# Performance work log

Hardware: AMD Instinct MI355X
Metric: run time of the kernel (lower is better)

Reference implementation:

```python
import jax, jax.numpy as jnp
import numpy as np

NEG_INF = -1e30  # masked_softmax fill (squad util convention)


def setup_inputs() -> dict:
    key = jax.random.key(0)
    ks = jax.random.split(key, 5)
    B, S, H = 4, 2048, 512
    x = jax.random.normal(ks[0], (B, S, H), dtype=jnp.float32)
    mask = jax.random.randint(ks[1], (B, S), 0, 2, dtype=jnp.int32)
    mask = mask.at[:, 0].set(1)  # ensure at least one valid key per row
    W_comb = jax.random.normal(ks[2], (H, 3 * H), dtype=jnp.float32) * (1.0 / np.sqrt(H))
    b_comb = jnp.zeros((3 * H,), dtype=jnp.float32)
    W_out = jax.random.normal(ks[3], (H, H), dtype=jnp.float32) * (1.0 / np.sqrt(H))
    b_out = jnp.zeros((H,), dtype=jnp.float32)
    return {"x": x, "mask": mask, "W_comb": W_comb, "b_comb": b_comb,
            "W_out": W_out, "b_out": b_out}


def reference(x, mask, W_comb, b_comb, W_out, b_out):
    B, S, H = x.shape
    n_head = 8
    d = H // n_head
    scale = d ** 0.5
    qkv = x @ W_comb + b_comb                      # [B,S,3H]
    q, k, v = jnp.split(qkv, 3, axis=-1)
    q = q.reshape(B, S, n_head, d)
    k = k.reshape(B, S, n_head, d)
    v = v.reshape(B, S, n_head, d)
    # [B,h,Sq,Sk] scores; mask applies along the key axis
    scores = jnp.einsum('bqhd,bkhd->bhqk', q / scale, k)
    key_mask = (mask > 0)[:, None, None, :]        # [B,1,1,Sk]
    logits = jnp.where(key_mask, scores, NEG_INF)
    attn = jax.nn.softmax(logits, axis=-1)         # dropout = identity (eval)
    out = jnp.einsum('bhqk,bkhd->bqhd', attn, v).reshape(B, S, H)
    return out @ W_out + b_out
```

## Files before the change

### kernel.cpp

```cpp
#include <hip/hip_runtime.h>
#include <hip/hip_bf16.h>
#include <stdint.h>

typedef unsigned short u16;
typedef unsigned int u32;
typedef __attribute__((ext_vector_type(8))) __bf16 bf16x8;
typedef __attribute__((ext_vector_type(8))) unsigned short us8;
typedef __attribute__((ext_vector_type(4))) unsigned short us4;
typedef __attribute__((ext_vector_type(4))) float f32x4;
typedef __attribute__((ext_vector_type(16))) float f32x16;
typedef __attribute__((ext_vector_type(4))) unsigned int u32x4;
typedef __attribute__((ext_vector_type(2))) unsigned int u32x2;

#define KSCALE_Q 0.18033688011112042f

#define VMCNT(n) asm volatile("s_waitcnt vmcnt(" #n ")" ::: "memory")
#define BARRIER() __builtin_amdgcn_s_barrier()

__device__ inline u16 f2bf(float f) {
  union { __bf16 b; u16 s; } x; x.b = (__bf16)f; return x.s;
}
__device__ inline u32 packbf(float a, float b) {
  return (u32)f2bf(a) | ((u32)f2bf(b) << 16);
}
__device__ inline f32x16 zero16() {
  f32x16 z; for (int i = 0; i < 16; ++i) z[i] = 0.f; return z;
}
__device__ __forceinline__ void gl_lds16(const u16* g, u16* l) {
  __builtin_amdgcn_global_load_lds(
      (const __attribute__((address_space(1))) void*)g,
      (__attribute__((address_space(3))) void*)l, 16, 0, 0);
}
__device__ __forceinline__ void pl32swap(u32& a, u32& b) {
#if __has_builtin(__builtin_amdgcn_permlane32_swap)
  u32x2 r = __builtin_amdgcn_permlane32_swap(a, b, false, false);
  a = r[0]; b = r[1];
#else
  u32 ta = (u32)__shfl_xor((int)a, 32);
  u32 tb = (u32)__shfl_xor((int)b, 32);
  int hi = (threadIdx.x & 63) >> 5;
  u32 na = hi ? tb : a;
  u32 nb = hi ? b : ta;
  a = na; b = nb;
#endif
}

__global__ __launch_bounds__(256) void prep(
    const float* __restrict__ x, const float* __restrict__ Wc,
    const float* __restrict__ Wo, const int* __restrict__ mask,
    u16* __restrict__ xbf, u16* __restrict__ wct, u16* __restrict__ wot,
    int* __restrict__ idx, int* __restrict__ nbv) {
  int r = blockIdx.x, tid = threadIdx.x;
  if (r < 4096) {
    int i = r * 256 + tid;
    float4 v = ((const float4*)x)[i];
    us4 o;
    o[0] = f2bf(v.x); o[1] = f2bf(v.y); o[2] = f2bf(v.z); o[3] = f2bf(v.w);
    ((us4*)xbf)[i] = o;
    return;
  }
  __shared__ float tile[32][33];
  __shared__ int ps[256];
  if (r < 5120) {
    const float* in; u16* outT; int R, C, bi;
    if (r < 4864) { in = Wc; outT = wct; R = 512; C = 1536; bi = r - 4096; }
    else          { in = Wo; outT = wot; R = 512; C = 512;  bi = r - 4864; }
    int nbx = C >> 5;
    int bx = bi % nbx, by = bi / nbx;
    int xq = tid & 31, yq = tid >> 5;
    int c0 = bx * 32, r0 = by * 32;
    for (int j = 0; j < 32; j += 8)
      tile[yq + j][xq] = in[(size_t)(r0 + yq + j) * C + c0 + xq];
    __syncthreads();
    for (int j = 0; j < 32; j += 8)
      outT[(size_t)(c0 + yq + j) * R + r0 + xq] = f2bf(tile[xq][yq + j]);
    return;
  }
  int b = r - 5120;
  const int* mrow = mask + b * 2048;
  int4 a = ((const int4*)mrow)[tid * 2];
  int4 c = ((const int4*)mrow)[tid * 2 + 1];
  int v[8] = {a.x, a.y, a.z, a.w, c.x, c.y, c.z, c.w};
  int cnt = 0;
  for (int i = 0; i < 8; ++i) cnt += (v[i] > 0);
  ps[tid] = cnt;
  __syncthreads();
  for (int off = 1; off < 256; off <<= 1) {
    int xv = ps[tid];
    int yv = (tid >= off) ? ps[tid - off] : 0;
    __syncthreads();
    ps[tid] = xv + yv;
    __syncthreads();
  }
  int total = ps[255];
  int pos = ps[tid] - cnt;
  int* ip = idx + b * 2048;
  for (int i = 0; i < 8; ++i)
    if (v[i] > 0) ip[pos++] = tid * 8 + i;
  for (int i = 0; i < 8; ++i) {
    int j = tid * 8 + i;
    if (j >= total) ip[j] = 0;
  }
  if (tid == 0) nbv[b] = total;
}

__global__ __launch_bounds__(256) void gemm_qkv(
    const u16* __restrict__ A, const u16* __restrict__ Bt,
    const float* __restrict__ bias, u16* __restrict__ Qc,
    u16* __restrict__ Kc, u16* __restrict__ VTc,
    const int* __restrict__ idx, const int* __restrict__ nbv) {
  const int K = 512;
  int bid = blockIdx.x;
  bool isQ = bid < 256;
  int b = 0, m0, n0;
  if (isQ) {
    m0 = (bid >> 2) * 128;
    n0 = (bid & 3) * 128;
  } else {
    int t = bid - 256;
    b = t >> 7;
    int rr_ = t & 127;
    m0 = (rr_ & 15) * 128;
    n0 = (rr_ >> 4) * 128 + 512;
    int npad = (nbv[b] + 127) & ~127;
    if (m0 >= npad) return;
  }
  __shared__ __align__(16) u16 As[2][128 * 64];
  __shared__ __align__(16) u16 Bs[2][128 * 64];
  int tid = threadIdx.x, wave = tid >> 6, lane = tid & 63;
  int quad = lane >> 4, l16 = lane & 15;
  int wm = (wave >> 1) * 64, wn = (wave & 1) * 64;

  int r8 = lane >> 3;
  int cb = (lane & 7) ^ r8;
  const u16* agp[4];
  for (int i = 0; i < 4; ++i) {
    int row = m0 + wave * 32 + i * 8 + r8;
    int grow = isQ ? row : (b * 2048 + idx[b * 2048 + row]);
    agp[i] = A + (size_t)grow * K + cb * 8;
  }
  const u16* bg = Bt + (size_t)(n0 + wave * 32 + r8) * K + cb * 8;
  int lofs = (wave * 32) * 64 + lane * 8;

  f32x4 acc[4][4];
  for (int i = 0; i < 4; ++i)
    for (int j = 0; j < 4; ++j) acc[i][j] = (f32x4){0.f, 0.f, 0.f, 0.f};

  int rx = l16 & 7;

  auto stage = [&](int buf, int kk) {
    u16* al = As[buf] + lofs;
    u16* bl = Bs[buf] + lofs;
#pragma unroll
    for (int i = 0; i < 4; ++i)
      gl_lds16(agp[i] + kk, al + i * 8 * 64);
#pragma unroll
    for (int i = 0; i < 4; ++i)
      gl_lds16(bg + kk + (size_t)(i * 8) * K, bl + i * 8 * 64);
  };

  stage(0, 0);
  for (int t = 0; t < 8; ++t) {
    if (t < 7) { stage((t + 1) & 1, (t + 1) * 64); VMCNT(8); }
    else       { VMCNT(0); }
    BARRIER();
    const u16* Asb = As[t & 1];
    const u16* Bsb = Bs[t & 1];
#pragma unroll
    for (int ks = 0; ks < 2; ++ks) {
      int pos = ((ks * 4 + quad) ^ rx) * 8;
      bf16x8 af[4], bfr[4];
#pragma unroll
      for (int i = 0; i < 4; ++i)
        af[i] = *(const bf16x8*)(Asb + (wm + i * 16 + l16) * 64 + pos);
#pragma unroll
      for (int j = 0; j < 4; ++j)
        bfr[j] = *(const bf16x8*)(Bsb + (wn + j * 16 + l16) * 64 + pos);
#pragma unroll
      for (int i = 0; i < 4; ++i)
#pragma unroll
        for (int j = 0; j < 4; ++j)
          acc[i][j] = __builtin_amdgcn_mfma_f32_16x16x32_bf16(
              af[i], bfr[j], acc[i][j], 0, 0, 0);
    }
    BARRIER();
  }
  for (int j = 0; j < 4; ++j) {
    int col = n0 + wn + j * 16 + l16;
    float bv = bias[col];
    if (isQ) {
      for (int i = 0; i < 4; ++i) {
        int rowb = m0 + wm + i * 16 + quad * 4;
        for (int rr = 0; rr < 4; ++rr)
          Qc[(size_t)(rowb + rr) * 512 + col] =
              f2bf((acc[i][j][rr] + bv) * KSCALE_Q);
      }
    } else if (col < 1024) {
      int ck = col - 512;
      for (int i = 0; i < 4; ++i) {
        int key0 = m0 + wm + i * 16 + quad * 4;
        for (int rr = 0; rr < 4; ++rr)
          Kc[((size_t)b * 2048 + key0 + rr) * 512 + ck] =
              f2bf(acc[i][j][rr] + bv);
      }
    } else {
      int hd = col - 1024;
      int h = hd >> 6, d = hd & 63;
      u16* vrow = VTc + ((size_t)(b * 8 + h) * 64 + d) * 2048;
      for (int i = 0; i < 4; ++i) {
        int key0 = m0 + wm + i * 16 + quad * 4;
        us4 pk;
        for (int rr = 0; rr < 4; ++rr) pk[rr] = f2bf(acc[i][j][rr] + bv);
        *(us4*)(vrow + key0) = pk;
      }
    }
  }
}

__global__ __launch_bounds__(256) void gemm_out(
    const u16* __restrict__ A, const u16* __restrict__ Bt,
    const float* __restrict__ bias, float* __restrict__ Cout) {
  const int K = 512, N = 512;
  int m0 = blockIdx.y * 128, n0 = blockIdx.x * 128;
  __shared__ __align__(16) u16 As[2][128 * 64];
  __shared__ __align__(16) u16 Bs[2][128 * 64];
  int tid = threadIdx.x, wave = tid >> 6, lane = tid & 63;
  int quad = lane >> 4, l16 = lane & 15;
  int wm = (wave >> 1) * 64, wn = (wave & 1) * 64;

  int r8 = lane >> 3;
  int cb = (lane & 7) ^ r8;
  const u16* ag = A + (size_t)(m0 + wave * 32 + r8) * K + cb * 8;
  const u16* bg = Bt + (size_t)(n0 + wave * 32 + r8) * K + cb * 8;
  int lofs = (wave * 32) * 64 + lane * 8;

  f32x4 acc[4][4];
  for (int i = 0; i < 4; ++i)
    for (int j = 0; j < 4; ++j) acc[i][j] = (f32x4){0.f, 0.f, 0.f, 0.f};

  int rx = l16 & 7;

  auto stage = [&](int buf, int kk) {
    u16* al = As[buf] + lofs;
    u16* bl = Bs[buf] + lofs;
#pragma unroll
    for (int i = 0; i < 4; ++i)
      gl_lds16(ag + kk + (size_t)(i * 8) * K, al + i * 8 * 64);
#pragma unroll
    for (int i = 0; i < 4; ++i)
      gl_lds16(bg + kk + (size_t)(i * 8) * K, bl + i * 8 * 64);
  };

  stage(0, 0);
  for (int t = 0; t < 8; ++t) {
    if (t < 7) { stage((t + 1) & 1, (t + 1) * 64); VMCNT(8); }
    else       { VMCNT(0); }
    BARRIER();
    const u16* Asb = As[t & 1];
    const u16* Bsb = Bs[t & 1];
#pragma unroll
    for (int ks = 0; ks < 2; ++ks) {
      int pos = ((ks * 4 + quad) ^ rx) * 8;
      bf16x8 af[4], bfr[4];
#pragma unroll
      for (int i = 0; i < 4; ++i)
        af[i] = *(const bf16x8*)(Asb + (wm + i * 16 + l16) * 64 + pos);
#pragma unroll
      for (int j = 0; j < 4; ++j)
        bfr[j] = *(const bf16x8*)(Bsb + (wn + j * 16 + l16) * 64 + pos);
#pragma unroll
      for (int i = 0; i < 4; ++i)
#pragma unroll
        for (int j = 0; j < 4; ++j)
          acc[i][j] = __builtin_amdgcn_mfma_f32_16x16x32_bf16(
              af[i], bfr[j], acc[i][j], 0, 0, 0);
    }
    BARRIER();
  }
  for (int j = 0; j < 4; ++j) {
    int col = n0 + wn + j * 16 + l16;
    float bv = bias[col];
    for (int i = 0; i < 4; ++i) {
      int rowb = m0 + wm + i * 16 + quad * 4;
      for (int rr = 0; rr < 4; ++rr)
        Cout[(size_t)(rowb + rr) * N + col] = acc[i][j][rr] + bv;
    }
  }
}

__global__ __launch_bounds__(256, 2) void attn_kernel(
    const u16* __restrict__ Qc, const u16* __restrict__ Kc,
    const u16* __restrict__ VTc, const int* __restrict__ nbv,
    u16* __restrict__ aout) {
  int flat = blockIdx.x;
  int xcd = flat & 7, ii = flat >> 3;
  int p = ((ii >> 4) << 3) | xcd;
  int c = ii & 15;
  int b = p >> 3, h = p & 7, q0 = c * 128;
  int bh = b * 8 + h;
  int tid = threadIdx.x, wave = tid >> 6, lane = tid & 63;
  int l5 = lane & 31, hi = lane >> 5;
  int nb = nbv[b];
  int npad = (nb + 127) & ~127;
  int NT = npad >> 7;

  __shared__ __align__(16) u16 Kt[2][128 * 64];
  __shared__ __align__(16) u16 Vt[2][64 * 128];

  bf16x8 qf[4];
  int qrow = b * 2048 + q0 + wave * 32 + l5;
#pragma unroll
  for (int s = 0; s < 4; ++s)
    qf[s] = *(const bf16x8*)(Qc + (size_t)qrow * 512 + h * 64 + s * 16 +
                             hi * 8);
  VMCNT(0);

  f32x16 o[2];
  o[0] = zero16(); o[1] = zero16();
  float lsum = 0.f;

  int krr = lane >> 3;
  int kcb = (lane & 7) ^ krr;
  const u16* kg = Kc + ((size_t)(b * 2048) + wave * 32 + krr) * 512 + h * 64 +
                  kcb * 8;
  int vrr = lane >> 4;

  auto stageKV = [&](int buf, int kt0) {
    u16* kl = Kt[buf] + (wave * 32) * 64 + lane * 8;
#pragma unroll
    for (int i = 0; i < 4; ++i)
      gl_lds16(kg + (size_t)(kt0 + i * 8) * 512, kl + i * 8 * 64);
    u16* vl = Vt[buf] + (wave * 16) * 128 + lane * 8;
#pragma unroll
    for (int i = 0; i < 4; ++i) {
      int vr = wave * 16 + i * 4 + vrr;
      int vcb = (lane & 15) ^ (vr & 15);
      gl_lds16(VTc + ((size_t)(bh * 64) + vr) * 2048 + kt0 + vcb * 8,
               vl + i * 4 * 128);
    }
  };

  int rx = l5 & 7;
  stageKV(0, 0);
  for (int t = 0; t < NT; ++t) {
    if (t + 1 < NT) { stageKV((t + 1) & 1, (t + 1) * 128); VMCNT(8); }
    else            { VMCNT(0); }
    BARRIER();
    const u16* Ktc = Kt[t & 1];
    const u16* Vtc = Vt[t & 1];
    int kt0 = t * 128;
    bool maskT = (kt0 + 128 > nb);

#pragma unroll
    for (int kp = 0; kp < 2; ++kp) {
      bf16x8 ka[2][4];
#pragma unroll
      for (int cc = 0; cc < 2; ++cc) {
        const u16* kro = Ktc + ((kp * 2 + cc) * 32 + l5) * 64;
#pragma unroll
        for (int s = 0; s < 4; ++s)
          ka[cc][s] = *(const bf16x8*)(kro + ((s * 2 + hi) ^ rx) * 8);
      }
      f32x16 sa[2];
      sa[0] = zero16(); sa[1] = zero16();
#pragma unroll
      for (int s = 0; s < 4; ++s) {
        sa[0] = __builtin_amdgcn_mfma_f32_32x32x16_bf16(ka[0][s], qf[s],
                                                        sa[0], 0, 0, 0);
        sa[1] = __builtin_amdgcn_mfma_f32_32x32x16_bf16(ka[1][s], qf[s],
                                                        sa[1], 0, 0, 0);
      }
      bf16x8 pb[2][2];
#pragma unroll
      for (int cc = 0; cc < 2; ++cc) {
        int kg4 = kp * 2 + cc;
        if (maskT) {
#pragma unroll
          for (int r = 0; r < 16; ++r) {
            int jg = kt0 + kg4 * 32 + (r & 3) + 8 * (r >> 2) + 4 * hi;
            if (jg >= nb) sa[cc][r] = -1e30f;
          }
        }
        u32 pk[8];
        float ls = 0.f;
#pragma unroll
        for (int j = 0; j < 8; ++j) {
          float e0 = __builtin_amdgcn_exp2f(sa[cc][2 * j]);
          float e1 = __builtin_amdgcn_exp2f(sa[cc][2 * j + 1]);
          ls += e0 + e1;
          pk[j] = packbf(e0, e1);
        }
        lsum += ls;
#pragma unroll
        for (int t2 = 0; t2 < 2; ++t2) {
          u32 a0 = pk[t2 * 4 + 0], a2 = pk[t2 * 4 + 2];
          u32 a1 = pk[t2 * 4 + 1], a3 = pk[t2 * 4 + 3];
          pl32swap(a0, a2);
          pl32swap(a1, a3);
          u32x4 qv; qv[0] = a0; qv[1] = a1; qv[2] = a2; qv[3] = a3;
          pb[cc][t2] = __builtin_bit_cast(bf16x8, qv);
        }
      }
#pragma unroll
      for (int cc = 0; cc < 2; ++cc) {
        int kg4 = kp * 2 + cc;
#pragma unroll
        for (int t2 = 0; t2 < 2; ++t2) {
          int cblk = kg4 * 4 + t2 * 2 + hi;
#pragma unroll
          for (int dc = 0; dc < 2; ++dc) {
            int vrow = dc * 32 + l5;
            bf16x8 va = *(const bf16x8*)(Vtc + vrow * 128 +
                                         ((cblk ^ (vrow & 15)) * 8));
            o[dc] = __builtin_amdgcn_mfma_f32_32x32x16_bf16(
                va, pb[cc][t2], o[dc], 0, 0, 0);
          }
        }
      }
    }
    BARRIER();
  }

  float lt = lsum;
  lt += __shfl_xor(lt, 32);
  float inv = 1.f / lt;
#pragma unroll
  for (int dc = 0; dc < 2; ++dc)
#pragma unroll
    for (int mI = 0; mI < 4; ++mI) {
      us4 pk;
      for (int r = 0; r < 4; ++r) pk[r] = f2bf(o[dc][mI * 4 + r] * inv);
      *(us4*)(aout + (size_t)qrow * 512 + h * 64 + dc * 32 + mI * 8 +
              hi * 4) = pk;
    }
}

extern "C" void kernel_launch(void* const* d_in, const int* in_sizes, int n_in,
                              void* d_out, int out_size, void* d_ws,
                              size_t ws_size, hipStream_t stream) {
  const float* x = (const float*)d_in[0];
  const int* mask = (const int*)d_in[1];
  const float* Wc = (const float*)d_in[2];
  const float* bc = (const float*)d_in[3];
  const float* Wo = (const float*)d_in[4];
  const float* bo = (const float*)d_in[5];
  float* out = (float*)d_out;

  char* ws = (char*)d_ws;
  u16* xbf = (u16*)(ws);
  u16* wct = (u16*)(ws + 8388608);
  u16* wot = (u16*)(ws + 9961472);
  u16* Qc  = (u16*)(ws + 10485760);
  u16* Kc  = (u16*)(ws + 18874368);
  u16* vtc = (u16*)(ws + 27262976);
  int* idx = (int*)(ws + 35651584);
  int* nbv = (int*)(ws + 35684352);
  u16* aout = xbf;

  prep<<<5124, 256, 0, stream>>>(x, Wc, Wo, mask, xbf, wct, wot, idx, nbv);
  gemm_qkv<<<768, 256, 0, stream>>>(xbf, wct, bc, Qc, Kc, vtc, idx, nbv);
  attn_kernel<<<512, 256, 0, stream>>>(Qc, Kc, vtc, nbv, aout);
  gemm_out<<<dim3(4, 64), 256, 0, stream>>>(aout, wot, bo, out);
}
```

Before: 144.2 us.

## Fuse prep, QKV GEMM, attention and output GEMM into one persistent kernel

Replaces the four separate launches with a single 512-block persistent kernel. The stages are separated by atomic-counter grid barriers. The QKV and output GEMM tiles are handed out through an atomic work queue, and shared memory is one buffer reused by every stage. The aim is to remove the launch gaps and tail drain between kernels, at the cost of spin-wait barriers, a memset of the counters, and a kernel that relies on all 512 blocks being co-resident under a two-blocks-per-CU register bound.

Result: slower. 462.5 us (+220.7%).

```diff
diff --git a/kernel.cpp b/kernel.cpp
--- a/kernel.cpp
+++ b/kernel.cpp
@@ -5,7 +5,6 @@
 typedef unsigned short u16;
 typedef unsigned int u32;
 typedef __attribute__((ext_vector_type(8))) __bf16 bf16x8;
-typedef __attribute__((ext_vector_type(8))) unsigned short us8;
 typedef __attribute__((ext_vector_type(4))) unsigned short us4;
 typedef __attribute__((ext_vector_type(4))) float f32x4;
 typedef __attribute__((ext_vector_type(16))) float f32x16;
@@ -13,6 +12,7 @@
 typedef __attribute__((ext_vector_type(2))) unsigned int u32x2;
 
 #define KSCALE_Q 0.18033688011112042f
+#define NBLK 512
 
 #define VMCNT(n) asm volatile("s_waitcnt vmcnt(" #n ")" ::: "memory")
 #define BARRIER() __builtin_amdgcn_s_barrier()
@@ -45,72 +45,28 @@
 #endif
 }
 
-__global__ __launch_bounds__(256) void prep(
-    const float* __restrict__ x, const float* __restrict__ Wc,
-    const float* __restrict__ Wo, const int* __restrict__ mask,
-    u16* __restrict__ xbf, u16* __restrict__ wct, u16* __restrict__ wot,
-    int* __restrict__ idx, int* __restrict__ nbv) {
-  int r = blockIdx.x, tid = threadIdx.x;
-  if (r < 4096) {
-    int i = r * 256 + tid;
-    float4 v = ((const float4*)x)[i];
-    us4 o;
-    o[0] = f2bf(v.x); o[1] = f2bf(v.y); o[2] = f2bf(v.z); o[3] = f2bf(v.w);
-    ((us4*)xbf)[i] = o;
-    return;
-  }
-  __shared__ float tile[32][33];
-  __shared__ int ps[256];
-  if (r < 5120) {
-    const float* in; u16* outT; int R, C, bi;
-    if (r < 4864) { in = Wc; outT = wct; R = 512; C = 1536; bi = r - 4096; }
-    else          { in = Wo; outT = wot; R = 512; C = 512;  bi = r - 4864; }
-    int nbx = C >> 5;
-    int bx = bi % nbx, by = bi / nbx;
-    int xq = tid & 31, yq = tid >> 5;
-    int c0 = bx * 32, r0 = by * 32;
-    for (int j = 0; j < 32; j += 8)
-      tile[yq + j][xq] = in[(size_t)(r0 + yq + j) * C + c0 + xq];
-    __syncthreads();
-    for (int j = 0; j < 32; j += 8)
-      outT[(size_t)(c0 + yq + j) * R + r0 + xq] = f2bf(tile[xq][yq + j]);
-    return;
-  }
-  int b = r - 5120;
-  const int* mrow = mask + b * 2048;
-  int4 a = ((const int4*)mrow)[tid * 2];
-  int4 c = ((const int4*)mrow)[tid * 2 + 1];
-  int v[8] = {a.x, a.y, a.z, a.w, c.x, c.y, c.z, c.w};
-  int cnt = 0;
-  for (int i = 0; i < 8; ++i) cnt += (v[i] > 0);
-  ps[tid] = cnt;
+__device__ __forceinline__ void grid_barrier(int* ctr) {
   __syncthreads();
-  for (int off = 1; off < 256; off <<= 1) {
-    int xv = ps[tid];
-    int yv = (tid >= off) ? ps[tid - off] : 0;
-    __syncthreads();
-    ps[tid] = xv + yv;
-    __syncthreads();
-  }
-  int total = ps[255];
-  int pos = ps[tid] - cnt;
-  int* ip = idx + b * 2048;
-  for (int i = 0; i < 8; ++i)
-    if (v[i] > 0) ip[pos++] = tid * 8 + i;
-  for (int i = 0; i < 8; ++i) {
-    int j = tid * 8 + i;
-    if (j >= total) ip[j] = 0;
-  }
-  if (tid == 0) nbv[b] = total;
-}
-
-__global__ __launch_bounds__(256) void gemm_qkv(
-    const u16* __restrict__ A, const u16* __restrict__ Bt,
+  if (threadIdx.x == 0) {
+    __hip_atomic_fetch_add(ctr, 1, __ATOMIC_RELEASE,
+                           __HIP_MEMORY_SCOPE_AGENT);
+    for (long sp = 0; sp < (1L << 26); ++sp) {
+      int v = __hip_atomic_load(ctr, __ATOMIC_ACQUIRE,
+                                __HIP_MEMORY_SCOPE_AGENT);
+      if (v >= NBLK) break;
+      __builtin_amdgcn_s_sleep(2);
+    }
+  }
+  __syncthreads();
+  __threadfence();
+}
+
+__device__ __forceinline__ void do_qkv(
+    int bid, const u16* __restrict__ A, const u16* __restrict__ Bt,
     const float* __restrict__ bias, u16* __restrict__ Qc,
     u16* __restrict__ Kc, u16* __restrict__ VTc,
-    const int* __restrict__ idx, const int* __restrict__ nbv) {
+    const int* __restrict__ idx, const int* __restrict__ nbv, u16* smem) {
   const int K = 512;
-  int bid = blockIdx.x;
   bool isQ = bid < 256;
   int b = 0, m0, n0;
   if (isQ) {
@@ -125,8 +81,8 @@
     int npad = (nbv[b] + 127) & ~127;
     if (m0 >= npad) return;
   }
-  __shared__ __align__(16) u16 As[2][128 * 64];
-  __shared__ __align__(16) u16 Bs[2][128 * 64];
+  u16* As = smem;
+  u16* Bs = smem + 16384;
   int tid = threadIdx.x, wave = tid >> 6, lane = tid & 63;
   int quad = lane >> 4, l16 = lane & 15;
   int wm = (wave >> 1) * 64, wn = (wave & 1) * 64;
@@ -149,8 +105,8 @@
   int rx = l16 & 7;
 
   auto stage = [&](int buf, int kk) {
-    u16* al = As[buf] + lofs;
-    u16* bl = Bs[buf] + lofs;
+    u16* al = As + buf * 8192 + lofs;
+    u16* bl = Bs + buf * 8192 + lofs;
 #pragma unroll
     for (int i = 0; i < 4; ++i)
       gl_lds16(agp[i] + kk, al + i * 8 * 64);
@@ -164,8 +120,8 @@
     if (t < 7) { stage((t + 1) & 1, (t + 1) * 64); VMCNT(8); }
     else       { VMCNT(0); }
     BARRIER();
-    const u16* Asb = As[t & 1];
-    const u16* Bsb = Bs[t & 1];
+    const u16* Asb = As + (t & 1) * 8192;
+    const u16* Bsb = Bs + (t & 1) * 8192;
 #pragma unroll
     for (int ks = 0; ks < 2; ++ks) {
       int pos = ((ks * 4 + quad) ^ rx) * 8;
@@ -217,82 +173,10 @@
   }
 }
 
-__global__ __launch_bounds__(256) void gemm_out(
-    const u16* __restrict__ A, const u16* __restrict__ Bt,
-    const float* __restrict__ bias, float* __restrict__ Cout) {
-  const int K = 512, N = 512;
-  int m0 = blockIdx.y * 128, n0 = blockIdx.x * 128;
-  __shared__ __align__(16) u16 As[2][128 * 64];
-  __shared__ __align__(16) u16 Bs[2][128 * 64];
-  int tid = threadIdx.x, wave = tid >> 6, lane = tid & 63;
-  int quad = lane >> 4, l16 = lane & 15;
-  int wm = (wave >> 1) * 64, wn = (wave & 1) * 64;
-
-  int r8 = lane >> 3;
-  int cb = (lane & 7) ^ r8;
-  const u16* ag = A + (size_t)(m0 + wave * 32 + r8) * K + cb * 8;
-  const u16* bg = Bt + (size_t)(n0 + wave * 32 + r8) * K + cb * 8;
-  int lofs = (wave * 32) * 64 + lane * 8;
-
-  f32x4 acc[4][4];
-  for (int i = 0; i < 4; ++i)
-    for (int j = 0; j < 4; ++j) acc[i][j] = (f32x4){0.f, 0.f, 0.f, 0.f};
-
-  int rx = l16 & 7;
-
-  auto stage = [&](int buf, int kk) {
-    u16* al = As[buf] + lofs;
-    u16* bl = Bs[buf] + lofs;
-#pragma unroll
-    for (int i = 0; i < 4; ++i)
-      gl_lds16(ag + kk + (size_t)(i * 8) * K, al + i * 8 * 64);
-#pragma unroll
-    for (int i = 0; i < 4; ++i)
-      gl_lds16(bg + kk + (size_t)(i * 8) * K, bl + i * 8 * 64);
-  };
-
-  stage(0, 0);
-  for (int t = 0; t < 8; ++t) {
-    if (t < 7) { stage((t + 1) & 1, (t + 1) * 64); VMCNT(8); }
-    else       { VMCNT(0); }
-    BARRIER();
-    const u16* Asb = As[t & 1];
-    const u16* Bsb = Bs[t & 1];
-#pragma unroll
-    for (int ks = 0; ks < 2; ++ks) {
-      int pos = ((ks * 4 + quad) ^ rx) * 8;
-      bf16x8 af[4], bfr[4];
-#pragma unroll
-      for (int i = 0; i < 4; ++i)
-        af[i] = *(const bf16x8*)(Asb + (wm + i * 16 + l16) * 64 + pos);
-#pragma unroll
-      for (int j = 0; j < 4; ++j)
-        bfr[j] = *(const bf16x8*)(Bsb + (wn + j * 16 + l16) * 64 + pos);
-#pragma unroll
-      for (int i = 0; i < 4; ++i)
-#pragma unroll
-        for (int j = 0; j < 4; ++j)
-          acc[i][j] = __builtin_amdgcn_mfma_f32_16x16x32_bf16(
-              af[i], bfr[j], acc[i][j], 0, 0, 0);
-    }
-    BARRIER();
-  }
-  for (int j = 0; j < 4; ++j) {
-    int col = n0 + wn + j * 16 + l16;
-    float bv = bias[col];
-    for (int i = 0; i < 4; ++i) {
-      int rowb = m0 + wm + i * 16 + quad * 4;
-      for (int rr = 0; rr < 4; ++rr)
-        Cout[(size_t)(rowb + rr) * N + col] = acc[i][j][rr] + bv;
-    }
-  }
-}
-
-__global__ __launch_bounds__(256, 2) void attn_kernel(
-    const u16* __restrict__ Qc, const u16* __restrict__ Kc,
+__device__ __forceinline__ void do_attn(
+    int flat, const u16* __restrict__ Qc, const u16* __restrict__ Kc,
     const u16* __restrict__ VTc, const int* __restrict__ nbv,
-    u16* __restrict__ aout) {
-  int flat = blockIdx.x;
+    u16* __restrict__ aout, u16* smem) {
   int xcd = flat & 7, ii = flat >> 3;
   int p = ((ii >> 4) << 3) | xcd;
   int c = ii & 15;
@@ -304,8 +188,8 @@
   int npad = (nb + 127) & ~127;
   int NT = npad >> 7;
 
-  __shared__ __align__(16) u16 Kt[2][128 * 64];
-  __shared__ __align__(16) u16 Vt[2][64 * 128];
+  u16* Kt = smem;
+  u16* Vt = smem + 16384;
 
   bf16x8 qf[4];
   int qrow = b * 2048 + q0 + wave * 32 + l5;
@@ -326,11 +210,11 @@
   int vrr = lane >> 4;
 
   auto stageKV = [&](int buf, int kt0) {
-    u16* kl = Kt[buf] + (wave * 32) * 64 + lane * 8;
+    u16* kl = Kt + buf * 8192 + (wave * 32) * 64 + lane * 8;
 #pragma unroll
     for (int i = 0; i < 4; ++i)
       gl_lds16(kg + (size_t)(kt0 + i * 8) * 512, kl + i * 8 * 64);
-    u16* vl = Vt[buf] + (wave * 16) * 128 + lane * 8;
+    u16* vl = Vt + buf * 8192 + (wave * 16) * 128 + lane * 8;
 #pragma unroll
     for (int i = 0; i < 4; ++i) {
       int vr = wave * 16 + i * 4 + vrr;
@@ -346,8 +230,8 @@
     if (t + 1 < NT) { stageKV((t + 1) & 1, (t + 1) * 128); VMCNT(8); }
     else            { VMCNT(0); }
     BARRIER();
-    const u16* Ktc = Kt[t & 1];
-    const u16* Vtc = Vt[t & 1];
+    const u16* Ktc = Kt + (t & 1) * 8192;
+    const u16* Vtc = Vt + (t & 1) * 8192;
     int kt0 = t * 128;
     bool maskT = (kt0 + 128 > nb);
 
@@ -433,6 +317,172 @@
       *(us4*)(aout + (size_t)qrow * 512 + h * 64 + dc * 32 + mI * 8 +
               hi * 4) = pk;
     }
+}
+
+__device__ __forceinline__ void do_out(
+    int job, const u16* __restrict__ A, const u16* __restrict__ Bt,
+    const float* __restrict__ bias, float* __restrict__ Cout, u16* smem) {
+  const int K = 512, N = 512;
+  int m0 = (job >> 2) * 128, n0 = (job & 3) * 128;
+  u16* As = smem;
+  u16* Bs = smem + 16384;
+  int tid = threadIdx.x, wave = tid >> 6, lane = tid & 63;
+  int quad = lane >> 4, l16 = lane & 15;
+  int wm = (wave >> 1) * 64, wn = (wave & 1) * 64;
+
+  int r8 = lane >> 3;
+  int cb = (lane & 7) ^ r8;
+  const u16* ag = A + (size_t)(m0 + wave * 32 + r8) * K + cb * 8;
+  const u16* bg = Bt + (size_t)(n0 + wave * 32 + r8) * K + cb * 8;
+  int lofs = (wave * 32) * 64 + lane * 8;
+
+  f32x4 acc[4][4];
+  for (int i = 0; i < 4; ++i)
+    for (int j = 0; j < 4; ++j) acc[i][j] = (f32x4){0.f, 0.f, 0.f, 0.f};
+
+  int rx = l16 & 7;
+
+  auto stage = [&](int buf, int kk) {
+    u16* al = As + buf * 8192 + lofs;
+    u16* bl = Bs + buf * 8192 + lofs;
+#pragma unroll
+    for (int i = 0; i < 4; ++i)
+      gl_lds16(ag + kk + (size_t)(i * 8) * K, al + i * 8 * 64);
+#pragma unroll
+    for (int i = 0; i < 4; ++i)
+      gl_lds16(bg + kk + (size_t)(i * 8) * K, bl + i * 8 * 64);
+  };
+
+  stage(0, 0);
+  for (int t = 0; t < 8; ++t) {
+    if (t < 7) { stage((t + 1) & 1, (t + 1) * 64); VMCNT(8); }
+    else       { VMCNT(0); }
+    BARRIER();
+    const u16* Asb = As + (t & 1) * 8192;
+    const u16* Bsb = Bs + (t & 1) * 8192;
+#pragma unroll
+    for (int ks = 0; ks < 2; ++ks) {
+      int pos = ((ks * 4 + quad) ^ rx) * 8;
+      bf16x8 af[4], bfr[4];
+#pragma unroll
+      for (int i = 0; i < 4; ++i)
+        af[i] = *(const bf16x8*)(Asb + (wm + i * 16 + l16) * 64 + pos);
+#pragma unroll
+      for (int j = 0; j < 4; ++j)
+        bfr[j] = *(const bf16x8*)(Bsb + (wn + j * 16 + l16) * 64 + pos);
+#pragma unroll
+      for (int i = 0; i < 4; ++i)
+#pragma unroll
+        for (int j = 0; j < 4; ++j)
+          acc[i][j] = __builtin_amdgcn_mfma_f32_16x16x32_bf16(
+              af[i], bfr[j], acc[i][j], 0, 0, 0);
+    }
+    BARRIER();
+  }
+  for (int j = 0; j < 4; ++j) {
+    int col = n0 + wn + j * 16 + l16;
+    float bv = bias[col];
+    for (int i = 0; i < 4; ++i) {
+      int rowb = m0 + wm + i * 16 + quad * 4;
+      for (int rr = 0; rr < 4; ++rr)
+        Cout[(size_t)(rowb + rr) * N + col] = acc[i][j][rr] + bv;
+    }
+  }
+}
+
+__global__ __launch_bounds__(256, 2) void fused(
+    const float* __restrict__ x, const float* __restrict__ Wc,
+    const float* __restrict__ Wo, const int* __restrict__ mask,
+    const float* __restrict__ bc, const float* __restrict__ bo,
+    u16* __restrict__ xbf, u16* __restrict__ wct, u16* __restrict__ wot,
+    u16* __restrict__ Qc, u16* __restrict__ Kc, u16* __restrict__ VTc,
+    int* __restrict__ idx, int* __restrict__ nbv, float* __restrict__ out,
+    int* __restrict__ ctrs) {
+  __shared__ __align__(16) u16 smem[32768];
+  __shared__ int jobS;
+  int tid = threadIdx.x, blk = blockIdx.x;
+
+  {
+#pragma unroll
+    for (int t = 0; t < 8; ++t) {
+      int i = blk * 2048 + t * 256 + tid;
+      float4 v = ((const float4*)x)[i];
+      us4 o;
+      o[0] = f2bf(v.x); o[1] = f2bf(v.y); o[2] = f2bf(v.z); o[3] = f2bf(v.w);
+      ((us4*)xbf)[i] = o;
+    }
+  }
+  {
+    float* tile = (float*)smem;
+    for (int tj = blk; tj < 1024; tj += NBLK) {
+      const float* in; u16* outT; int R, C, bi;
+      if (tj < 768) { in = Wc; outT = wct; R = 512; C = 1536; bi = tj; }
+      else          { in = Wo; outT = wot; R = 512; C = 512;  bi = tj - 768; }
+      int nbx = C >> 5;
+      int bx = bi % nbx, by = bi / nbx;
+      int xq = tid & 31, yq = tid >> 5;
+      int c0 = bx * 32, r0 = by * 32;
+      for (int j = 0; j < 32; j += 8)
+        tile[(yq + j) * 33 + xq] = in[(size_t)(r0 + yq + j) * C + c0 + xq];
+      __syncthreads();
+      for (int j = 0; j < 32; j += 8)
+        outT[(size_t)(c0 + yq + j) * R + r0 + xq] =
+            f2bf(tile[xq * 33 + yq + j]);
+      __syncthreads();
+    }
+  }
+  if (blk < 4) {
+    int* ps = (int*)(smem + 4096);
+    int b = blk;
+    const int* mrow = mask + b * 2048;
+    int4 a = ((const int4*)mrow)[tid * 2];
+    int4 c = ((const int4*)mrow)[tid * 2 + 1];
+    int v[8] = {a.x, a.y, a.z, a.w, c.x, c.y, c.z, c.w};
+    int cnt = 0;
+    for (int i = 0; i < 8; ++i) cnt += (v[i] > 0);
+    ps[tid] = cnt;
+    __syncthreads();
+    for (int off = 1; off < 256; off <<= 1) {
+      int xv = ps[tid];
+      int yv = (tid >= off) ? ps[tid - off] : 0;
+      __syncthreads();
+      ps[tid] = xv + yv;
+      __syncthreads();
+    }
+    int total = ps[255];
+    int pos = ps[tid] - cnt;
+    int* ip = idx + b * 2048;
+    for (int i = 0; i < 8; ++i)
+      if (v[i] > 0) ip[pos++] = tid * 8 + i;
+    for (int i = 0; i < 8; ++i) {
+      int j = tid * 8 + i;
+      if (j >= total) ip[j] = 0;
+    }
+    if (tid == 0) nbv[b] = total;
+  }
+  grid_barrier(ctrs + 0);
+
+  for (;;) {
+    __syncthreads();
+    if (tid == 0) jobS = atomicAdd(ctrs + 4, 1);
+    __syncthreads();
+    int job = jobS;
+    if (job >= 768) break;
+    do_qkv(job, xbf, wct, bc, Qc, Kc, VTc, idx, nbv, smem);
+  }
+  grid_barrier(ctrs + 1);
+
+  do_attn(blk, Qc, Kc, VTc, nbv, xbf , smem);
+  grid_barrier(ctrs + 2);
+
+  for (;;) {
+    __syncthreads();
+    if (tid == 0) jobS = atomicAdd(ctrs + 5, 1);
+    __syncthreads();
+    int job = jobS;
+    if (job >= 256) break;
+    do_out(job, xbf, wot, bo, out, smem);
+  }
 }
 
 extern "C" void kernel_launch(void* const* d_in, const int* in_sizes, int n_in,
@@ -455,10 +505,9 @@
   u16* vtc = (u16*)(ws + 27262976);
   int* idx = (int*)(ws + 35651584);
   int* nbv = (int*)(ws + 35684352);
-  u16* aout = xbf;
-
-  prep<<<5124, 256, 0, stream>>>(x, Wc, Wo, mask, xbf, wct, wot, idx, nbv);
-  gemm_qkv<<<768, 256, 0, stream>>>(xbf, wct, bc, Qc, Kc, vtc, idx, nbv);
-  attn_kernel<<<512, 256, 0, stream>>>(Qc, Kc, vtc, nbv, aout);
-  gemm_out<<<dim3(4, 64), 256, 0, stream>>>(aout, wot, bo, out);
-}
+  int* ctrs = (int*)(ws + 35684416);
+
+  hipMemsetAsync(ctrs, 0, 32, stream);
+  fused<<<NBLK, 256, 0, stream>>>(x, Wc, Wo, mask, bc, bo, xbf, wct, wot,
+                                  Qc, Kc, vtc, idx, nbv, out, ctrs);
+}
```

## Halve attention KV tile to 64 keys, raise occupancy, split output GEMM tiles

Applied to the files above, without the earlier changes.

The attention kernel now stages 64-key K/V tiles instead of 128, which halves LDS per block, and raises launch bounds to allow 4 blocks per CU. It also wraps the MFMA sections in s_setprio so waves doing matrix work get priority. The output GEMM switches to 128x64 tiles on a 512-block 1D grid so more CUs are busy. The costs are more loop iterations and barriers per key and more A-tile reloads in the GEMM.

Result: slower. 148.9 us (+3.3%).

```diff
diff --git a/kernel.cpp b/kernel.cpp
--- a/kernel.cpp
+++ b/kernel.cpp
@@ -5,7 +5,6 @@
 typedef unsigned short u16;
 typedef unsigned int u32;
 typedef __attribute__((ext_vector_type(8))) __bf16 bf16x8;
-typedef __attribute__((ext_vector_type(8))) unsigned short us8;
 typedef __attribute__((ext_vector_type(4))) unsigned short us4;
 typedef __attribute__((ext_vector_type(4))) float f32x4;
 typedef __attribute__((ext_vector_type(16))) float f32x16;
@@ -217,43 +216,45 @@
   }
 }
 
-__global__ __launch_bounds__(256) void gemm_out(
+__global__ __launch_bounds__(256, 3) void gemm_out(
     const u16* __restrict__ A, const u16* __restrict__ Bt,
     const float* __restrict__ bias, float* __restrict__ Cout) {
   const int K = 512, N = 512;
-  int m0 = blockIdx.y * 128, n0 = blockIdx.x * 128;
+  int bid = blockIdx.x;
+  int m0 = (bid >> 3) * 128, n0 = (bid & 7) * 64;
   __shared__ __align__(16) u16 As[2][128 * 64];
-  __shared__ __align__(16) u16 Bs[2][128 * 64];
+  __shared__ __align__(16) u16 Bs[2][64 * 64];
   int tid = threadIdx.x, wave = tid >> 6, lane = tid & 63;
   int quad = lane >> 4, l16 = lane & 15;
-  int wm = (wave >> 1) * 64, wn = (wave & 1) * 64;
+  int wm = (wave >> 1) * 64, wn = (wave & 1) * 32;
 
   int r8 = lane >> 3;
   int cb = (lane & 7) ^ r8;
   const u16* ag = A + (size_t)(m0 + wave * 32 + r8) * K + cb * 8;
-  const u16* bg = Bt + (size_t)(n0 + wave * 32 + r8) * K + cb * 8;
-  int lofs = (wave * 32) * 64 + lane * 8;
-
-  f32x4 acc[4][4];
+  const u16* bg = Bt + (size_t)(n0 + wave * 16 + r8) * K + cb * 8;
+  int lofsA = (wave * 32) * 64 + lane * 8;
+  int lofsB = (wave * 16) * 64 + lane * 8;
+
+  f32x4 acc[4][2];
   for (int i = 0; i < 4; ++i)
-    for (int j = 0; j < 4; ++j) acc[i][j] = (f32x4){0.f, 0.f, 0.f, 0.f};
+    for (int j = 0; j < 2; ++j) acc[i][j] = (f32x4){0.f, 0.f, 0.f, 0.f};
 
   int rx = l16 & 7;
 
   auto stage = [&](int buf, int kk) {
-    u16* al = As[buf] + lofs;
-    u16* bl = Bs[buf] + lofs;
+    u16* al = As[buf] + lofsA;
+    u16* bl = Bs[buf] + lofsB;
 #pragma unroll
     for (int i = 0; i < 4; ++i)
       gl_lds16(ag + kk + (size_t)(i * 8) * K, al + i * 8 * 64);
 #pragma unroll
-    for (int i = 0; i < 4; ++i)
+    for (int i = 0; i < 2; ++i)
       gl_lds16(bg + kk + (size_t)(i * 8) * K, bl + i * 8 * 64);
   };
 
   stage(0, 0);
   for (int t = 0; t < 8; ++t) {
-    if (t < 7) { stage((t + 1) & 1, (t + 1) * 64); VMCNT(8); }
+    if (t < 7) { stage((t + 1) & 1, (t + 1) * 64); VMCNT(6); }
     else       { VMCNT(0); }
     BARRIER();
     const u16* Asb = As[t & 1];
@@ -261,23 +262,23 @@
 #pragma unroll
     for (int ks = 0; ks < 2; ++ks) {
       int pos = ((ks * 4 + quad) ^ rx) * 8;
-      bf16x8 af[4], bfr[4];
+      bf16x8 af[4], bfr[2];
 #pragma unroll
       for (int i = 0; i < 4; ++i)
         af[i] = *(const bf16x8*)(Asb + (wm + i * 16 + l16) * 64 + pos);
 #pragma unroll
-      for (int j = 0; j < 4; ++j)
+      for (int j = 0; j < 2; ++j)
         bfr[j] = *(const bf16x8*)(Bsb + (wn + j * 16 + l16) * 64 + pos);
 #pragma unroll
       for (int i = 0; i < 4; ++i)
 #pragma unroll
-        for (int j = 0; j < 4; ++j)
+        for (int j = 0; j < 2; ++j)
           acc[i][j] = __builtin_amdgcn_mfma_f32_16x16x32_bf16(
               af[i], bfr[j], acc[i][j], 0, 0, 0);
     }
     BARRIER();
   }
-  for (int j = 0; j < 4; ++j) {
+  for (int j = 0; j < 2; ++j) {
     int col = n0 + wn + j * 16 + l16;
     float bv = bias[col];
     for (int i = 0; i < 4; ++i) {
@@ -288,7 +289,7 @@
   }
 }
 
-__global__ __launch_bounds__(256, 2) void attn_kernel(
+__global__ __launch_bounds__(256, 4) void attn_kernel(
     const u16* __restrict__ Qc, const u16* __restrict__ Kc,
     const u16* __restrict__ VTc, const int* __restrict__ nbv,
     u16* __restrict__ aout) {
@@ -301,11 +302,10 @@
   int tid = threadIdx.x, wave = tid >> 6, lane = tid & 63;
   int l5 = lane & 31, hi = lane >> 5;
   int nb = nbv[b];
-  int npad = (nb + 127) & ~127;
-  int NT = npad >> 7;
-
-  __shared__ __align__(16) u16 Kt[2][128 * 64];
-  __shared__ __align__(16) u16 Vt[2][64 * 128];
+  int NT = ((nb + 63) & ~63) >> 6;
+
+  __shared__ __align__(16) u16 Kt[2][64 * 64];
+  __shared__ __align__(16) u16 Vt[2][64 * 64];
 
   bf16x8 qf[4];
   int qrow = b * 2048 + q0 + wave * 32 + l5;
@@ -319,105 +319,98 @@
   o[0] = zero16(); o[1] = zero16();
   float lsum = 0.f;
 
-  int krr = lane >> 3;
-  int kcb = (lane & 7) ^ krr;
-  const u16* kg = Kc + ((size_t)(b * 2048) + wave * 32 + krr) * 512 + h * 64 +
-                  kcb * 8;
-  int vrr = lane >> 4;
+  int rr8 = lane >> 3;
+  int cb8 = (lane & 7) ^ rr8;
+  const u16* kg = Kc + ((size_t)(b * 2048) + wave * 16 + rr8) * 512 + h * 64 +
+                  cb8 * 8;
+  const u16* vg = VTc + ((size_t)(bh * 64) + wave * 16 + rr8) * 2048 + cb8 * 8;
 
   auto stageKV = [&](int buf, int kt0) {
-    u16* kl = Kt[buf] + (wave * 32) * 64 + lane * 8;
-#pragma unroll
-    for (int i = 0; i < 4; ++i)
-      gl_lds16(kg + (size_t)(kt0 + i * 8) * 512, kl + i * 8 * 64);
-    u16* vl = Vt[buf] + (wave * 16) * 128 + lane * 8;
-#pragma unroll
-    for (int i = 0; i < 4; ++i) {
-      int vr = wave * 16 + i * 4 + vrr;
-      int vcb = (lane & 15) ^ (vr & 15);
-      gl_lds16(VTc + ((size_t)(bh * 64) + vr) * 2048 + kt0 + vcb * 8,
-               vl + i * 4 * 128);
-    }
+    u16* kl = Kt[buf] + (wave * 16) * 64 + lane * 8;
+    gl_lds16(kg + (size_t)kt0 * 512, kl);
+    gl_lds16(kg + (size_t)(kt0 + 8) * 512, kl + 8 * 64);
+    u16* vl = Vt[buf] + (wave * 16) * 64 + lane * 8;
+    gl_lds16(vg + kt0, vl);
+    gl_lds16(vg + kt0 + (size_t)8 * 2048, vl + 8 * 64);
   };
 
   int rx = l5 & 7;
   stageKV(0, 0);
   for (int t = 0; t < NT; ++t) {
-    if (t + 1 < NT) { stageKV((t + 1) & 1, (t + 1) * 128); VMCNT(8); }
+    if (t + 1 < NT) { stageKV((t + 1) & 1, (t + 1) * 64); VMCNT(4); }
     else            { VMCNT(0); }
     BARRIER();
     const u16* Ktc = Kt[t & 1];
     const u16* Vtc = Vt[t & 1];
-    int kt0 = t * 128;
-    bool maskT = (kt0 + 128 > nb);
-
-#pragma unroll
-    for (int kp = 0; kp < 2; ++kp) {
-      bf16x8 ka[2][4];
-#pragma unroll
-      for (int cc = 0; cc < 2; ++cc) {
-        const u16* kro = Ktc + ((kp * 2 + cc) * 32 + l5) * 64;
-#pragma unroll
-        for (int s = 0; s < 4; ++s)
-          ka[cc][s] = *(const bf16x8*)(kro + ((s * 2 + hi) ^ rx) * 8);
-      }
-      f32x16 sa[2];
-      sa[0] = zero16(); sa[1] = zero16();
-#pragma unroll
-      for (int s = 0; s < 4; ++s) {
-        sa[0] = __builtin_amdgcn_mfma_f32_32x32x16_bf16(ka[0][s], qf[s],
-                                                        sa[0], 0, 0, 0);
-        sa[1] = __builtin_amdgcn_mfma_f32_32x32x16_bf16(ka[1][s], qf[s],
-                                                        sa[1], 0, 0, 0);
-      }
-      bf16x8 pb[2][2];
-#pragma unroll
-      for (int cc = 0; cc < 2; ++cc) {
-        int kg4 = kp * 2 + cc;
-        if (maskT) {
-#pragma unroll
-          for (int r = 0; r < 16; ++r) {
-            int jg = kt0 + kg4 * 32 + (r & 3) + 8 * (r >> 2) + 4 * hi;
-            if (jg >= nb) sa[cc][r] = -1e30f;
-          }
+    int kt0 = t * 64;
+    bool maskT = (kt0 + 64 > nb);
+
+    bf16x8 ka[2][4];
+#pragma unroll
+    for (int cc = 0; cc < 2; ++cc) {
+      const u16* kro = Ktc + (cc * 32 + l5) * 64;
+#pragma unroll
+      for (int s = 0; s < 4; ++s)
+        ka[cc][s] = *(const bf16x8*)(kro + (((s * 2 + hi) ^ rx) * 8));
+    }
+    f32x16 sa[2];
+    sa[0] = zero16(); sa[1] = zero16();
+    __builtin_amdgcn_s_setprio(1);
+#pragma unroll
+    for (int s = 0; s < 4; ++s) {
+      sa[0] = __builtin_amdgcn_mfma_f32_32x32x16_bf16(ka[0][s], qf[s],
+                                                      sa[0], 0, 0, 0);
+      sa[1] = __builtin_amdgcn_mfma_f32_32x32x16_bf16(ka[1][s], qf[s],
+                                                      sa[1], 0, 0, 0);
+    }
+    __builtin_amdgcn_s_setprio(0);
+    bf16x8 pb[2][2];
+#pragma unroll
+    for (int cc = 0; cc < 2; ++cc) {
+      if (maskT) {
+#pragma unroll
+        for (int r = 0; r < 16; ++r) {
+          int jg = kt0 + cc * 32 + (r & 3) + 8 * (r >> 2) + 4 * hi;
+          if (jg >= nb) sa[cc][r] = -1e30f;
         }
-        u32 pk[8];
-        float ls = 0.f;
-#pragma unroll
-        for (int j = 0; j < 8; ++j) {
-          float e0 = __builtin_amdgcn_exp2f(sa[cc][2 * j]);
-          float e1 = __builtin_amdgcn_exp2f(sa[cc][2 * j + 1]);
-          ls += e0 + e1;
-          pk[j] = packbf(e0, e1);
+      }
+      u32 pk[8];
+      float ls = 0.f;
+#pragma unroll
+      for (int j = 0; j < 8; ++j) {
+        float e0 = __builtin_amdgcn_exp2f(sa[cc][2 * j]);
+        float e1 = __builtin_amdgcn_exp2f(sa[cc][2 * j + 1]);
+        ls += e0 + e1;
+        pk[j] = packbf(e0, e1);
+      }
+      lsum += ls;
+#pragma unroll
+      for (int t2 = 0; t2 < 2; ++t2) {
+        u32 a0 = pk[t2 * 4 + 0], a2 = pk[t2 * 4 + 2];
+        u32 a1 = pk[t2 * 4 + 1], a3 = pk[t2 * 4 + 3];
+        pl32swap(a0, a2);
+        pl32swap(a1, a3);
+        u32x4 qv; qv[0] = a0; qv[1] = a1; qv[2] = a2; qv[3] = a3;
+        pb[cc][t2] = __builtin_bit_cast(bf16x8, qv);
+      }
+    }
+    __builtin_amdgcn_s_setprio(1);
+#pragma unroll
+    for (int cc = 0; cc < 2; ++cc) {
+#pragma unroll
+      for (int t2 = 0; t2 < 2; ++t2) {
+        int cblk = cc * 4 + t2 * 2 + hi;
+#pragma unroll
+        for (int dc = 0; dc < 2; ++dc) {
+          int vrow = dc * 32 + l5;
+          bf16x8 va = *(const bf16x8*)(Vtc + vrow * 64 +
+                                       ((cblk ^ (vrow & 7)) * 8));
+          o[dc] = __builtin_amdgcn_mfma_f32_32x32x16_bf16(
+              va, pb[cc][t2], o[dc], 0, 0, 0);
         }
-        lsum += ls;
-#pragma unroll
-        for (int t2 = 0; t2 < 2; ++t2) {
-          u32 a0 = pk[t2 * 4 + 0], a2 = pk[t2 * 4 + 2];
-          u32 a1 = pk[t2 * 4 + 1], a3 = pk[t2 * 4 + 3];
-          pl32swap(a0, a2);
-          pl32swap(a1, a3);
-          u32x4 qv; qv[0] = a0; qv[1] = a1; qv[2] = a2; qv[3] = a3;
-          pb[cc][t2] = __builtin_bit_cast(bf16x8, qv);
-        }
-      }
-#pragma unroll
-      for (int cc = 0; cc < 2; ++cc) {
-        int kg4 = kp * 2 + cc;
-#pragma unroll
-        for (int t2 = 0; t2 < 2; ++t2) {
-          int cblk = kg4 * 4 + t2 * 2 + hi;
-#pragma unroll
-          for (int dc = 0; dc < 2; ++dc) {
-            int vrow = dc * 32 + l5;
-            bf16x8 va = *(const bf16x8*)(Vtc + vrow * 128 +
-                                         ((cblk ^ (vrow & 15)) * 8));
-            o[dc] = __builtin_amdgcn_mfma_f32_32x32x16_bf16(
-                va, pb[cc][t2], o[dc], 0, 0, 0);
-          }
-        }
-      }
-    }
+      }
+    }
+    __builtin_amdgcn_s_setprio(0);
     BARRIER();
   }
 
@@ -460,5 +453,5 @@
   prep<<<5124, 256, 0, stream>>>(x, Wc, Wo, mask, xbf, wct, wot, idx, nbv);
   gemm_qkv<<<768, 256, 0, stream>>>(xbf, wct, bc, Qc, Kc, vtc, idx, nbv);
   attn_kernel<<<512, 256, 0, stream>>>(Qc, Kc, vtc, nbv, aout);
-  gemm_out<<<dim3(4, 64), 256, 0, stream>>>(aout, wot, bo, out);
-}
+  gemm_out<<<512, 256, 0, stream>>>(aout, wot, bo, out);
+}
```
